# Optimization experiments

Measured on AMD Instinct MI355X. Metric: run time of the kernel, lower is better.

The kernel has to match this reference:

```python
import jax, jax.numpy as jnp
import numpy as np

N_QUBIT = 16
N_LAYERS = 4


def _rx(t):
    # RX(t) = [[cos(t/2), -i sin(t/2)], [-i sin(t/2), cos(t/2)]]; t: scalar or (B,)
    c = jnp.cos(t * 0.5) + 0j
    s = -1j * jnp.sin(t * 0.5)
    return jnp.stack([jnp.stack([c, s], -1), jnp.stack([s, c], -1)], -2)


def _ry(t):
    c = jnp.cos(t * 0.5) + 0j
    s = jnp.sin(t * 0.5) + 0j
    return jnp.stack([jnp.stack([c, -s], -1), jnp.stack([s, c], -1)], -2)


def _rz(t):
    p = jnp.exp(-0.5j * t)
    z = jnp.zeros_like(p)
    return jnp.stack([jnp.stack([p, z], -1), jnp.stack([z, jnp.conj(p)], -1)], -2)


def _apply_1q(state, U, wire, n):
    # state: (B, 2**n); U: (2,2) shared or (B,2,2) per-sample. Wire 0 = MSB.
    B = state.shape[0]
    L, R = 2 ** wire, 2 ** (n - wire - 1)
    s = state.reshape(B, L, 2, R)
    if U.ndim == 3:
        s = jnp.einsum('bij,bljr->blir', U, s)
    else:
        s = jnp.einsum('ij,bljr->blir', U, s)
    return s.reshape(B, 2 ** n)


def _apply_cnot(state, c, t, n):
    # CNOT control c, target t (flip target where control bit = 1)
    B = state.shape[0]
    a, b = (c, t) if c < t else (t, c)
    L, M, R = 2 ** a, 2 ** (b - a - 1), 2 ** (n - b - 1)
    s = state.reshape(B, L, 2, M, 2, R)
    if c < t:
        s0 = s[:, :, 0]                       # (B, L, M, 2, R)
        s1 = jnp.flip(s[:, :, 1], axis=3)     # flip target bit
        s = jnp.stack([s0, s1], axis=2)
    else:
        s0 = s[:, :, :, :, 0]                 # (B, L, 2, M, R)
        s1 = jnp.flip(s[:, :, :, :, 1], axis=2)
        s = jnp.stack([s0, s1], axis=4)
    return s.reshape(B, 2 ** n)


def setup_inputs() -> dict:
    key = jax.random.key(0)
    k1, k2 = jax.random.split(key)
    X = jax.random.normal(k1, (512, N_QUBIT), dtype=jnp.float32)
    weights = (np.pi * jax.random.uniform(k2, (N_LAYERS, N_QUBIT, 3))).astype(jnp.float32)
    bias = jnp.zeros((1,), dtype=jnp.float32)
    return {"X": X, "weights": weights, "bias": bias}


def reference(X, weights, bias):
    B, n = X.shape
    state = jnp.zeros((B, 2 ** n), jnp.complex64).at[:, 0].set(1.0)
    enc_angles = 2.0 * jnp.arctan(X)  # (B, n)
    for l in range(N_LAYERS):
        # encoder: RX(2*arctan(x_w)) on wire w (per-sample angles)
        for w in range(n):
            state = _apply_1q(state, _rx(enc_angles[:, w]), w, n)
        # single StronglyEntanglingLayers layer: Rot(phi,theta,omega) = RZ(phi) -> RY(theta) -> RZ(omega)
        for w in range(n):
            state = _apply_1q(state, _rz(weights[l, w, 0]), w, n)
            state = _apply_1q(state, _ry(weights[l, w, 1]), w, n)
            state = _apply_1q(state, _rz(weights[l, w, 2]), w, n)
        # entangler: ring of CNOTs with range r=1 (single-layer default)
        for w in range(n):
            state = _apply_cnot(state, w, (w + 1) % n, n)
    # <Z_0>: wire 0 is the most significant bit
    probs = jnp.abs(state.reshape(B, 2, -1)) ** 2
    z = probs[:, 0].sum(-1) - probs[:, 1].sum(-1)  # (B,)
    return z[:, None].astype(jnp.float32) + bias   # (B, 1), matches torch.stack of (scalar + bias)
```

## Files before the change

### kernel.cpp

```cpp
#include <hip/hip_runtime.h>
#include <hip/hip_fp16.h>
#include <cstdint>
#include <cstring>


struct BundleMeta {
    uint16_t voff[16];
    uint16_t row[4];
    uint16_t flip[4];
    uint8_t  piv[4];
    uint8_t  gidx[4];
    uint8_t  nl[4];
};

struct PassMeta {
    int       nbundles;
    BundleMeta bd[24];
    uint8_t   gap[4];
    uint8_t   nlw[4];
    uint8_t   wire_of_bit[12];
    uint16_t  meas_row;
    uint8_t   meas_nl;
};

struct Sched { int np; PassMeta pms[8]; };

constexpr Sched build_sched() {
    Sched S{};
    const int MAXP = 8;
    uint16_t D[16]{}, R[16]{};
    for (int w = 0; w < 16; ++w) { D[w] = R[w] = (uint16_t)(1u << w); }
    uint16_t gD[48]{}, gR[48]{}; uint8_t ggi[48]{}; bool gk[48]{};
    int ng = 0;
    for (int l = 1; l <= 3; ++l) {
        for (int w = 0; w < 16; ++w) { int t = (w + 1) & 15; D[w] ^= D[t]; R[t] ^= R[w]; }
        for (int w = 0; w < 16; ++w) {
            gD[ng] = D[w]; gR[ng] = R[w]; ggi[ng] = (uint8_t)(l * 16 + w);
            gk[ng] = true; ++ng;
        }
    }
    for (int w = 0; w < 16; ++w) { int t = (w + 1) & 15; D[w] ^= D[t]; R[t] ^= R[w]; }
    const uint16_t Rmeas = R[0];
    {
        uint16_t keptD[49]{}, keptR[49]{}; int nk = 0;
        keptD[nk] = 0; keptR[nk] = Rmeas; ++nk;
        for (int i = ng - 1; i >= 0; --i) {
            bool comm = true;
            for (int k = 0; k < nk; ++k) {
                if (__builtin_parity((unsigned)(gD[i] & keptR[k])) ||
                    __builtin_parity((unsigned)(keptD[k] & gR[i]))) { comm = false; break; }
            }
            if (comm) gk[i] = false;
            else { keptD[nk] = gD[i]; keptR[nk] = gR[i]; ++nk; }
        }
    }
    int nkept = 0; unsigned long long keptM = 0;
    for (int i = 0; i < ng; ++i) if (gk[i]) { ++nkept; keptM |= 1ull << i; }
    unsigned long long cm[48]{};
    for (int i = 0; i < ng; ++i)
        for (int j = 0; j < ng; ++j)
            if (!(__builtin_parity((unsigned)(gD[i] & gR[j])) ||
                  __builtin_parity((unsigned)(gD[j] & gR[i]))))
                cm[i] |= 1ull << j;
    int passOf[48]{};
    for (int i = 0; i < ng; ++i) passOf[i] = -1;
    auto bitsim = [&](uint16_t SA_, uint16_t SB_, int maxnp, int* po) -> int {
        unsigned long long sc = 0; int rem = nkept, npp = 0, stall = 0;
        while (rem > 0 && npp < MAXP) {
            uint16_t Sm = (npp & 1) ? SB_ : SA_;
            int got = 0;
            for (int i = 0; i < ng; ++i) {
                unsigned long long bi = 1ull << i;
                if (!(keptM & bi) || (sc & bi)) continue;
                if (gD[i] & Sm) continue;
                unsigned long long prior = keptM & ~sc & (bi - 1ull);
                if (prior & ~cm[i]) continue;
                sc |= bi; --rem; ++got;
                if (po) po[i] = npp;
            }
            ++npp;
            if (!got) { if (++stall >= 2) break; } else stall = 0;
            if (rem > 0 && npp >= maxnp) return 99;
        }
        return rem == 0 ? npp : 99;
    };
    int bestA = -1, bestB = 0;
    for (int target = 2; target <= MAXP && bestA < 0; ++target)
        for (int a = 0; a < 16 && bestA < 0; ++a)
            for (int b = 0; b < 16; ++b) {
                uint16_t SA_ = 0, SB_ = 0;
                for (int k = 0; k < 4; ++k) {
                    SA_ |= (uint16_t)(1u << ((a + k) & 15));
                    SB_ |= (uint16_t)(1u << ((b + k) & 15));
                }
                int rv = bitsim(SA_, SB_, target, nullptr);
                if (rv <= target) { bestA = a; bestB = b; break; }
            }
    if (bestA < 0) { bestA = 0; bestB = 8; }
    uint16_t SA = 0, SB = 0;
    int exA[4]{}, exB[4]{};
    for (int k = 0; k < 4; ++k) {
        exA[k] = (bestA + k) & 15; exB[k] = (bestB + k) & 15;
        SA |= (uint16_t)(1u << exA[k]); SB |= (uint16_t)(1u << exB[k]);
    }
    int np = bitsim(SA, SB, MAXP, passOf);
    if (np > MAXP) np = MAXP;
    if (np < 2) np = 2;
    int wireToPos[16]{}; bool used[16]{};
    int pos = 15;
    for (int k = 0; k < 4; ++k) { wireToPos[exA[k]] = pos--; used[exA[k]] = true; }
    for (int k = 0; k < 4; ++k)
        if (!used[exB[k]]) { wireToPos[exB[k]] = pos--; used[exB[k]] = true; }
    for (int w = 0; w < 16; ++w) if (!used[w]) wireToPos[w] = pos--;
    int posToWire[16]{};
    for (int w = 0; w < 16; ++w) posToWire[wireToPos[w]] = w;
    for (int p = 0; p < np; ++p) {
        PassMeta& M = S.pms[p];
        const int* ex = (p & 1) ? exB : exA;
        int gp[4]{}, gw[4]{};
        for (int k = 0; k < 4; ++k) { gp[k] = wireToPos[ex[k]]; gw[k] = ex[k]; }
        for (int a2 = 0; a2 < 4; ++a2)
            for (int b2 = a2 + 1; b2 < 4; ++b2)
                if (gp[b2] < gp[a2]) {
                    int t = gp[a2]; gp[a2] = gp[b2]; gp[b2] = t;
                    t = gw[a2]; gw[a2] = gw[b2]; gw[b2] = t;
                }
        for (int k = 0; k < 4; ++k) { M.gap[k] = (uint8_t)gp[k]; M.nlw[k] = (uint8_t)gw[k]; }
        int packedOfWire[16]{};
        for (int w = 0; w < 16; ++w) packedOfWire[w] = -1;
        int t = 0;
        for (int q = 0; q < 16; ++q) {
            bool isgap = false;
            for (int k = 0; k < 4; ++k) if (q == gp[k]) isgap = true;
            if (isgap) continue;
            M.wire_of_bit[t] = (uint8_t)posToWire[q];
            packedOfWire[posToWire[q]] = t;
            ++t;
        }
        uint16_t lm[48]{}, lr[48]{}; uint8_t lnl[48]{}, lgx[48]{}; int nsel = 0;
        for (int i = 0; i < ng; ++i) {
            if (!gk[i] || passOf[i] != p) continue;
            uint16_t m = 0, r = 0; uint8_t nl = 0;
            for (int w = 0; w < 16; ++w) {
                if ((gD[i] >> w) & 1) m |= (uint16_t)(1u << packedOfWire[w]);
                if (((gR[i] >> w) & 1) && packedOfWire[w] >= 0)
                    r |= (uint16_t)(1u << packedOfWire[w]);
            }
            for (int k = 0; k < 4; ++k)
                if ((gR[i] >> gw[k]) & 1) nl |= (uint8_t)(1u << k);
            lm[nsel] = m; lr[nsel] = r; lnl[nsel] = nl; lgx[nsel] = ggi[i]; ++nsel;
        }
        M.nbundles = 0;
        int s = 0;
        while (s < nsel && M.nbundles < 24) {
            BundleMeta& B = M.bd[M.nbundles]; ++M.nbundles;
            for (int j = 0; j < 4; ++j) {
                B.gidx[j] = 0xFF; B.row[j] = 0; B.flip[j] = 0; B.nl[j] = 0;
            }
            uint16_t red[4]{}, om[4]{}; int pv[4]{}; int nsl = 0;
            while (nsl < 4 && s < nsel) {
                uint16_t r0 = lm[s];
                for (int j = 0; j < nsl; ++j)
                    if ((r0 >> pv[j]) & 1) r0 ^= red[j];
                if (!r0) break;
                pv[nsl] = 31 - __builtin_clz((unsigned)r0);
                red[nsl] = r0; om[nsl] = lm[s];
                B.gidx[nsl] = lgx[s]; B.row[nsl] = lr[s]; B.nl[nsl] = lnl[s];
                ++nsl; ++s;
            }
            for (int b = 11; b >= 0 && nsl < 4; --b) {
                uint16_t r0 = (uint16_t)(1u << b);
                for (int j = 0; j < nsl; ++j)
                    if ((r0 >> pv[j]) & 1) r0 ^= red[j];
                if (!r0) continue;
                pv[nsl] = 31 - __builtin_clz((unsigned)r0);
                red[nsl] = r0; om[nsl] = (uint16_t)(1u << b);
                ++nsl;
            }
            for (int tt = 0; tt < 16; ++tt) {
                uint16_t v = 0;
                for (int j = 0; j < 4; ++j) if ((tt >> j) & 1) v ^= om[j];
                B.voff[tt] = v;
            }
            for (int j = 0; j < 4; ++j) {
                if (B.gidx[j] == 0xFF) continue;
                uint16_t f = 0;
                for (int tt = 0; tt < 16; ++tt)
                    if (__builtin_parity((unsigned)(B.voff[tt] & B.row[j])))
                        f |= (uint16_t)(1u << tt);
                B.flip[j] = f;
            }
            for (int a2 = 0; a2 < 4; ++a2)
                for (int b2 = a2 + 1; b2 < 4; ++b2)
                    if (pv[b2] < pv[a2]) { int tt = pv[a2]; pv[a2] = pv[b2]; pv[b2] = tt; }
            for (int j = 0; j < 4; ++j) B.piv[j] = (uint8_t)pv[j];
        }
        {
            uint16_t r = 0; uint8_t nl = 0;
            for (int w = 0; w < 16; ++w)
                if (((Rmeas >> w) & 1) && packedOfWire[w] >= 0)
                    r |= (uint16_t)(1u << packedOfWire[w]);
            for (int k = 0; k < 4; ++k)
                if ((Rmeas >> gw[k]) & 1) nl |= (uint8_t)(1u << k);
            M.meas_row = r; M.meas_nl = nl;
        }
    }
    S.np = np;
    return S;
}

constexpr Sched SCHED = build_sched();

typedef _Float16 h2 __attribute__((ext_vector_type(2)));

__device__ __forceinline__ float2 cmul2(float2 a, float2 b) {
    return make_float2(a.x * b.x - a.y * b.y, a.x * b.y + a.y * b.x);
}
__device__ __forceinline__ h2 pkfma(h2 a, h2 b, h2 c) {
    return __builtin_bit_cast(h2, __hfma2(__builtin_bit_cast(__half2, a),
                                          __builtin_bit_cast(__half2, b),
                                          __builtin_bit_cast(__half2, c)));
}
__device__ __forceinline__ h2 h2x(h2 a, unsigned m) {
    return __builtin_bit_cast(h2, __builtin_bit_cast(unsigned, a) ^ m);
}
__device__ __forceinline__ h2 bch2(unsigned u) { return __builtin_bit_cast(h2, u); }
__device__ __forceinline__ float xorf(float a, unsigned s) {
    return __uint_as_float(__float_as_uint(a) ^ s);
}
__device__ __forceinline__ unsigned pkh2(float lo, float hi) {
    h2 v; v.x = (_Float16)lo; v.y = (_Float16)hi;
    return __builtin_bit_cast(unsigned, v);
}

__device__ __forceinline__ void pair_rot(unsigned& np_, unsigned& nq_,
    unsigned p, unsigned q, unsigned AR, unsigned AIt, unsigned BRt, unsigned BI)
{
    unsigned a, b;
    asm("v_pk_mul_f16 %0, %1, %3\n\t"
        "v_pk_fma_f16 %0, %2, %3, %0 op_sel:[0,1,0] op_sel_hi:[1,0,1] neg_lo:[1,0,0]\n\t"
        "v_pk_fma_f16 %0, %4, %5, %0\n\t"
        "v_pk_fma_f16 %0, %6, %5, %0 op_sel:[0,1,0] op_sel_hi:[1,0,1] neg_lo:[1,0,0]"
        : "=&v"(a)
        : "v"(AR), "v"(AIt), "v"(p), "v"(BRt), "v"(q), "v"(BI));
    asm("v_pk_mul_f16 %0, %1, %5\n\t"
        "v_pk_fma_f16 %0, %2, %5, %0 op_sel:[0,1,0] op_sel_hi:[1,0,1] neg_hi:[1,0,0]\n\t"
        "v_pk_fma_f16 %0, %4, %3, %0 neg_lo:[1,0,0] neg_hi:[1,0,0]\n\t"
        "v_pk_fma_f16 %0, %6, %3, %0 op_sel:[0,1,0] op_sel_hi:[1,0,1] neg_lo:[1,0,0]"
        : "=&v"(b)
        : "v"(AR), "v"(AIt), "v"(p), "v"(BRt), "v"(q), "v"(BI));
    np_ = a; nq_ = b;
}

__global__ __launch_bounds__(512)
void precompute_kernel(const float* __restrict__ X, const float* __restrict__ Wt,
                       const float* __restrict__ Bs, uint4* __restrict__ Ug,
                       float* __restrict__ out)
{
    int id = blockIdx.x * 512 + threadIdx.x;
    if (id >= 512 * 64) return;
    int b = id >> 6, lw = id & 63, l = lw >> 4, w = lw & 15;
    float x  = X[b * 16 + w];
    float ce = 1.0f / sqrtf(1.0f + x * x);
    float se = x * ce;
    float t0 = 0.5f * Wt[(l * 16 + w) * 3 + 0];
    float t1 = 0.5f * Wt[(l * 16 + w) * 3 + 1];
    float t2 = 0.5f * Wt[(l * 16 + w) * 3 + 2];
    float c1 = cosf(t1), s1 = sinf(t1);
    float ca = cosf(t0 + t2), sa = sinf(t0 + t2);
    float cb = cosf(t2 - t0), sb = sinf(t2 - t0);
    float2 W00 = make_float2( c1 * ca, -c1 * sa);
    float2 W01 = make_float2(-s1 * cb,  s1 * sb);
    float2 a  = make_float2(W00.x * ce + W01.y * se, W00.y * ce - W01.x * se);
    float2 bb = make_float2(W00.y * se + W01.x * ce, -W00.x * se + W01.y * ce);
    uint4 o;
    o.x = pkh2(a.x,  a.x);
    o.y = pkh2(a.y,  a.y);
    o.z = pkh2(bb.x, bb.x);
    o.w = pkh2(bb.y, bb.y);
    Ug[id] = o;
    if (lw == 0) out[b] = Bs[0];
}

template <int P>
__global__ __launch_bounds__(256, 8)
void pass_kernel(const uint4* __restrict__ Ug, unsigned* __restrict__ state,
                 float* __restrict__ out)
{
    static constexpr PassMeta M = SCHED.pms[P];
    constexpr int NP   = SCHED.np;
    constexpr int MODE = (P == 0) ? 0 : ((P == NP - 1) ? 2 : 1);

    __shared__ __align__(16) unsigned amp[4096];
    __shared__ uint4 coef[64];
    const int tid = threadIdx.x;
    const int bb  = blockIdx.x >> 4;
    const unsigned c = blockIdx.x & 15u;
    const size_t base = (size_t)bb << 16;
    if (tid < 64) coef[tid] = Ug[(size_t)bb * 64 + tid];

    auto expand = [&](unsigned x) -> unsigned {
        #pragma unroll
        for (int k = 0; k < 4; ++k) {
            const unsigned g = M.gap[k];
            x = ((x >> g) << (g + 1)) | (x & ((1u << g) - 1u)) | (((c >> k) & 1u) << g);
        }
        return x;
    };

    if constexpr (MODE == 0) {
        __syncthreads();
        if (tid == 0) {
            float2 kv = make_float2(1.f, 0.f);
            #pragma unroll
            for (int t = 0; t < 4; ++t) {
                uint4 u = coef[M.nlw[t]];
                float ar = (float)bch2(u.x).x, ai = (float)bch2(u.y).x;
                float br = (float)bch2(u.z).x, bi = (float)bch2(u.w).x;
                float2 col = ((c >> t) & 1u) ? make_float2(-br, bi)
                                             : make_float2(ar, ai);
                kv = cmul2(kv, col);
            }
            amp[0] = pkh2(kv.x, kv.y);
        }
        __syncthreads();
        #pragma unroll
        for (int s = 0; s < 12; ++s) {
            const int n = 1 << s;
            uint4 cf = coef[M.wire_of_bit[s]];
            const h2 AR2  = bch2(cf.x);
            const h2 AIpm = h2x(bch2(cf.y), 0x00008000u);
            const h2 BRn  = h2x(bch2(cf.z), 0x80008000u);
            const h2 BIpm = h2x(bch2(cf.w), 0x00008000u);
            for (int i = tid; i < n; i += 256) {
                h2 a = bch2(amp[i]);
                h2 sw = a.yx;
                amp[i + n] = __builtin_bit_cast(unsigned, pkfma(BRn, a, BIpm * sw));
                amp[i]     = __builtin_bit_cast(unsigned, pkfma(AR2, a, AIpm * sw));
            }
            __syncthreads();
        }
    } else {
        #pragma unroll
        for (int it = 0; it < 4; ++it) {
            unsigned u = (unsigned)(tid + it * 256) * 4u;
            unsigned a = expand(u);
            uint4 v = *reinterpret_cast<const uint4*>(state + base + a);
            *reinterpret_cast<uint4*>(&amp[u]) = v;
        }
        __syncthreads();
    }

    #pragma unroll
    for (int ci = 0; ci < M.nbundles; ++ci) {
        unsigned r = (unsigned)tid;
        #pragma unroll
        for (int k = 0; k < 4; ++k) {
            const unsigned p = M.bd[ci].piv[k];
            r = ((r >> p) << (p + 1)) | (r & ((1u << p) - 1u));
        }
        const unsigned rb = r << 2;
        unsigned a_[16];
        #pragma unroll
        for (int t = 0; t < 16; ++t)
            a_[t] = *(const unsigned*)((const char*)amp +
                     (rb ^ ((unsigned)M.bd[ci].voff[t] << 2)));
        #pragma unroll
        for (int g = 0; g < 4; ++g) {
            if (M.bd[ci].gidx[g] == 0xFF) continue;
            const uint4 cf = coef[M.bd[ci].gidx[g]];
            const unsigned par = ((unsigned)__popc(r & (unsigned)M.bd[ci].row[g]) +
                                  (unsigned)__popc((unsigned)M.bd[ci].nl[g] & c)) & 1u;
            const unsigned gm = par ? 0x80008000u : 0u;
            const unsigned AR  = cf.x;
            const unsigned BI  = cf.w;
            const unsigned AIg = cf.y ^ gm;
            const unsigned BRg = cf.z ^ gm;
            const unsigned AIf = AIg ^ 0x80008000u;
            const unsigned BRf = BRg ^ 0x80008000u;
            #pragma unroll
            for (int t = 0; t < 16; ++t) {
                if (t & (1 << g)) continue;
                const int t2 = t | (1 << g);
                const bool FB = ((M.bd[ci].flip[g] >> t) & 1u) != 0;
                unsigned np_, nq_;
                pair_rot(np_, nq_, a_[t], a_[t2], AR,
                         FB ? AIf : AIg, FB ? BRf : BRg, BI);
                a_[t] = np_; a_[t2] = nq_;
            }
        }
        if (MODE == 2 && ci == M.nbundles - 1) {
            float acc = 0.f;
            const unsigned sb = (((unsigned)__popc(r & (unsigned)M.meas_row) +
                                  (unsigned)__popc((unsigned)M.meas_nl & c)) & 1u) << 31;
            #pragma unroll
            for (int t = 0; t < 16; ++t) {
                h2 a = bch2(a_[t]);
                float vr = (float)a.x, vi = (float)a.y;
                float pr = __builtin_fmaf(vr, vr, vi * vi);
                const unsigned st =
                    __builtin_parity((unsigned)(M.bd[ci].voff[t] & M.meas_row))
                        ? 0x80000000u : 0u;
                acc += xorf(pr, sb ^ st);
            }
            for (int off = 32; off > 0; off >>= 1) acc += __shfl_down(acc, off, 64);
            if ((tid & 63) == 0) atomicAdd(&out[bb], acc);
            return;
        }
        #pragma unroll
        for (int t = 0; t < 16; ++t)
            *(unsigned*)((char*)amp + (rb ^ ((unsigned)M.bd[ci].voff[t] << 2))) = a_[t];
        __syncthreads();
    }

    if constexpr (MODE == 2) {
        float acc = 0.f;
        const unsigned mcp = (unsigned)(__popc((unsigned)M.meas_nl & c) & 1);
        for (int k = 0; k < 16; ++k) {
            unsigned u = (unsigned)(tid + k * 256);
            h2 a = bch2(amp[u]);
            float vr = (float)a.x, vi = (float)a.y;
            float pr = __builtin_fmaf(vr, vr, vi * vi);
            acc += (((unsigned)__popc(u & (unsigned)M.meas_row) & 1u) ^ mcp)
                 ? -pr : pr;
        }
        for (int off = 32; off > 0; off >>= 1) acc += __shfl_down(acc, off, 64);
        if ((tid & 63) == 0) atomicAdd(&out[bb], acc);
    } else {
        #pragma unroll
        for (int it = 0; it < 4; ++it) {
            unsigned u = (unsigned)(tid + it * 256) * 4u;
            unsigned ad = expand(u);
            uint4 v = *reinterpret_cast<const uint4*>(&amp[u]);
            *reinterpret_cast<uint4*>(state + base + ad) = v;
        }
    }
}

extern "C" void kernel_launch(void* const* d_in, const int* in_sizes, int n_in,
                              void* d_out, int out_size, void* d_ws, size_t ws_size,
                              hipStream_t stream)
{
    const float* X  = (const float*)d_in[0];
    const float* Wt = (const float*)d_in[1];
    const float* Bs = (const float*)d_in[2];
    float* out = (float*)d_out;

    const size_t UG_BYTES = (size_t)512 * 64 * sizeof(uint4);
    uint4*    Ug    = (uint4*)d_ws;
    unsigned* state = (unsigned*)((char*)d_ws + UG_BYTES);
    size_t avail = ws_size > UG_BYTES ? ws_size - UG_BYTES : 0;
    int group = 1;
    while (group < 512 && (size_t)(group * 2) * 262144ull <= avail)
        group <<= 1;
    const int ngroups = 512 / group;

    constexpr int NP = SCHED.np;

    precompute_kernel<<<dim3(64), dim3(512), 0, stream>>>(X, Wt, Bs, Ug, out);
    for (int g = 0; g < ngroups; ++g) {
        const uint4* ug = Ug + (size_t)g * group * 64;
        float* og = out + (size_t)g * group;
        dim3 grid((unsigned)(group << 4));
        for (int p = 0; p < NP; ++p) {
            switch (p) {
            case 0: pass_kernel<0><<<grid, dim3(256), 0, stream>>>(ug, state, og); break;
            case 1: pass_kernel<1><<<grid, dim3(256), 0, stream>>>(ug, state, og); break;
            case 2: pass_kernel<2><<<grid, dim3(256), 0, stream>>>(ug, state, og); break;
            case 3: pass_kernel<3><<<grid, dim3(256), 0, stream>>>(ug, state, og); break;
            case 4: pass_kernel<4><<<grid, dim3(256), 0, stream>>>(ug, state, og); break;
            case 5: pass_kernel<5><<<grid, dim3(256), 0, stream>>>(ug, state, og); break;
            case 6: pass_kernel<6><<<grid, dim3(256), 0, stream>>>(ug, state, og); break;
            case 7: pass_kernel<7><<<grid, dim3(256), 0, stream>>>(ug, state, og); break;
            }
        }
    }

    (void)in_sizes; (void)n_in; (void)out_size; (void)ws_size;
}
```

Before: 330.1 us.

## Pack more gates per register bundle and build initial product state in parallel

```diff
diff --git a/kernel.cpp b/kernel.cpp
--- a/kernel.cpp
+++ b/kernel.cpp
@@ -4,18 +4,26 @@
 #include <cstring>
 
 
+struct GateC {
+    uint16_t row;
+    uint16_t flip;
+    uint8_t  mt;
+    uint8_t  nl;
+    uint8_t  gidx;
+    uint8_t  pad;
+};
+
 struct BundleMeta {
     uint16_t voff[16];
-    uint16_t row[4];
-    uint16_t flip[4];
     uint8_t  piv[4];
-    uint8_t  gidx[4];
-    uint8_t  nl[4];
+    uint8_t  ngates;
+    uint8_t  pad[3];
+    GateC    gc[24];
 };
 
 struct PassMeta {
     int       nbundles;
-    BundleMeta bd[24];
+    BundleMeta bd[8];
     uint8_t   gap[4];
     uint8_t   nlw[4];
     uint8_t   wire_of_bit[12];
@@ -151,49 +159,57 @@
             lm[nsel] = m; lr[nsel] = r; lnl[nsel] = nl; lgx[nsel] = ggi[i]; ++nsel;
         }
         M.nbundles = 0;
-        int s = 0;
-        while (s < nsel && M.nbundles < 24) {
+        int i = 0;
+        while (i < nsel && M.nbundles < 8) {
             BundleMeta& B = M.bd[M.nbundles]; ++M.nbundles;
-            for (int j = 0; j < 4; ++j) {
-                B.gidx[j] = 0xFF; B.row[j] = 0; B.flip[j] = 0; B.nl[j] = 0;
-            }
-            uint16_t red[4]{}, om[4]{}; int pv[4]{}; int nsl = 0;
-            while (nsl < 4 && s < nsel) {
-                uint16_t r0 = lm[s];
-                for (int j = 0; j < nsl; ++j)
-                    if ((r0 >> pv[j]) & 1) r0 ^= red[j];
-                if (!r0) break;
-                pv[nsl] = 31 - __builtin_clz((unsigned)r0);
-                red[nsl] = r0; om[nsl] = lm[s];
-                B.gidx[nsl] = lgx[s]; B.row[nsl] = lr[s]; B.nl[nsl] = lnl[s];
-                ++nsl; ++s;
-            }
-            for (int b = 11; b >= 0 && nsl < 4; --b) {
-                uint16_t r0 = (uint16_t)(1u << b);
-                for (int j = 0; j < nsl; ++j)
-                    if ((r0 >> pv[j]) & 1) r0 ^= red[j];
-                if (!r0) continue;
-                pv[nsl] = 31 - __builtin_clz((unsigned)r0);
-                red[nsl] = r0; om[nsl] = (uint16_t)(1u << b);
-                ++nsl;
+            uint16_t om[4]{}, red[4]{}; int pv[4]{}; uint8_t comb[4]{};
+            int rank = 0, ngate = 0;
+            while (i < nsel && ngate < 24) {
+                uint16_t x = lm[i]; uint8_t rep = 0;
+                for (int j = 0; j < rank; ++j)
+                    if ((x >> pv[j]) & 1) { x ^= red[j]; rep ^= comb[j]; }
+                if (x == 0) {
+                    B.gc[ngate].mt = rep;
+                    B.gc[ngate].row = lr[i]; B.gc[ngate].nl = lnl[i];
+                    B.gc[ngate].gidx = lgx[i];
+                    ++ngate; ++i;
+                } else if (rank < 4) {
+                    om[rank] = lm[i]; red[rank] = x;
+                    pv[rank] = 31 - __builtin_clz((unsigned)x);
+                    comb[rank] = (uint8_t)((1u << rank) | rep);
+                    B.gc[ngate].mt = (uint8_t)(1u << rank);
+                    B.gc[ngate].row = lr[i]; B.gc[ngate].nl = lnl[i];
+                    B.gc[ngate].gidx = lgx[i];
+                    ++ngate; ++i; ++rank;
+                } else break;
+            }
+            B.ngates = (uint8_t)ngate;
+            for (int b = 11; b >= 0 && rank < 4; --b) {
+                uint16_t x = (uint16_t)(1u << b);
+                for (int j = 0; j < rank; ++j)
+                    if ((x >> pv[j]) & 1) x ^= red[j];
+                if (!x) continue;
+                om[rank] = (uint16_t)(1u << b); red[rank] = x;
+                pv[rank] = 31 - __builtin_clz((unsigned)x);
+                ++rank;
             }
             for (int tt = 0; tt < 16; ++tt) {
                 uint16_t v = 0;
                 for (int j = 0; j < 4; ++j) if ((tt >> j) & 1) v ^= om[j];
                 B.voff[tt] = v;
             }
-            for (int j = 0; j < 4; ++j) {
-                if (B.gidx[j] == 0xFF) continue;
+            for (int g2 = 0; g2 < ngate; ++g2) {
                 uint16_t f = 0;
                 for (int tt = 0; tt < 16; ++tt)
-                    if (__builtin_parity((unsigned)(B.voff[tt] & B.row[j])))
+                    if (__builtin_parity((unsigned)(B.voff[tt] & B.gc[g2].row)))
                         f |= (uint16_t)(1u << tt);
-                B.flip[j] = f;
-            }
+                B.gc[g2].flip = f;
+            }
+            int sp[4] = {pv[0], pv[1], pv[2], pv[3]};
             for (int a2 = 0; a2 < 4; ++a2)
                 for (int b2 = a2 + 1; b2 < 4; ++b2)
-                    if (pv[b2] < pv[a2]) { int tt = pv[a2]; pv[a2] = pv[b2]; pv[b2] = tt; }
-            for (int j = 0; j < 4; ++j) B.piv[j] = (uint8_t)pv[j];
+                    if (sp[b2] < sp[a2]) { int tt = sp[a2]; sp[a2] = sp[b2]; sp[b2] = tt; }
+            for (int j = 0; j < 4; ++j) B.piv[j] = (uint8_t)sp[j];
         }
         {
             uint16_t r = 0; uint8_t nl = 0;
@@ -310,22 +326,29 @@
 
     if constexpr (MODE == 0) {
         __syncthreads();
-        if (tid == 0) {
-            float2 kv = make_float2(1.f, 0.f);
-            #pragma unroll
-            for (int t = 0; t < 4; ++t) {
-                uint4 u = coef[M.nlw[t]];
-                float ar = (float)bch2(u.x).x, ai = (float)bch2(u.y).x;
-                float br = (float)bch2(u.z).x, bi = (float)bch2(u.w).x;
-                float2 col = ((c >> t) & 1u) ? make_float2(-br, bi)
-                                             : make_float2(ar, ai);
-                kv = cmul2(kv, col);
-            }
-            amp[0] = pkh2(kv.x, kv.y);
-        }
+        float2 kv = make_float2(1.f, 0.f);
+        #pragma unroll
+        for (int t = 0; t < 4; ++t) {
+            uint4 u = coef[M.nlw[t]];
+            float ar = (float)bch2(u.x).x, ai = (float)bch2(u.y).x;
+            float br = (float)bch2(u.z).x, bi = (float)bch2(u.w).x;
+            float2 col = ((c >> t) & 1u) ? make_float2(-br, bi)
+                                         : make_float2(ar, ai);
+            kv = cmul2(kv, col);
+        }
+        #pragma unroll
+        for (int b = 0; b < 8; ++b) {
+            uint4 u = coef[M.wire_of_bit[b]];
+            float ar = (float)bch2(u.x).x, ai = (float)bch2(u.y).x;
+            float br = (float)bch2(u.z).x, bi = (float)bch2(u.w).x;
+            float2 col = (((unsigned)tid >> b) & 1u) ? make_float2(-br, bi)
+                                                     : make_float2(ar, ai);
+            kv = cmul2(kv, col);
+        }
+        amp[tid] = pkh2(kv.x, kv.y);
         __syncthreads();
         #pragma unroll
-        for (int s = 0; s < 12; ++s) {
+        for (int s = 8; s < 12; ++s) {
             const int n = 1 << s;
             uint4 cf = coef[M.wire_of_bit[s]];
             const h2 AR2  = bch2(cf.x);
@@ -366,11 +389,11 @@
             a_[t] = *(const unsigned*)((const char*)amp +
                      (rb ^ ((unsigned)M.bd[ci].voff[t] << 2)));
         #pragma unroll
-        for (int g = 0; g < 4; ++g) {
-            if (M.bd[ci].gidx[g] == 0xFF) continue;
-            const uint4 cf = coef[M.bd[ci].gidx[g]];
-            const unsigned par = ((unsigned)__popc(r & (unsigned)M.bd[ci].row[g]) +
-                                  (unsigned)__popc((unsigned)M.bd[ci].nl[g] & c)) & 1u;
+        for (int gi = 0; gi < M.bd[ci].ngates; ++gi) {
+            const uint4 cf = coef[M.bd[ci].gc[gi].gidx];
+            const unsigned par =
+                ((unsigned)__popc(r & (unsigned)M.bd[ci].gc[gi].row) +
+                 (unsigned)__popc((unsigned)M.bd[ci].gc[gi].nl & c)) & 1u;
             const unsigned gm = par ? 0x80008000u : 0u;
             const unsigned AR  = cf.x;
             const unsigned BI  = cf.w;
@@ -378,11 +401,13 @@
             const unsigned BRg = cf.z ^ gm;
             const unsigned AIf = AIg ^ 0x80008000u;
             const unsigned BRf = BRg ^ 0x80008000u;
+            const int mt = M.bd[ci].gc[gi].mt;
+            const int mh = 1 << (31 - __builtin_clz((unsigned)mt));
             #pragma unroll
             for (int t = 0; t < 16; ++t) {
-                if (t & (1 << g)) continue;
-                const int t2 = t | (1 << g);
-                const bool FB = ((M.bd[ci].flip[g] >> t) & 1u) != 0;
+                if (t & mh) continue;
+                const int t2 = t ^ mt;
+                const bool FB = ((M.bd[ci].gc[gi].flip >> t) & 1u) != 0;
                 unsigned np_, nq_;
                 pair_rot(np_, nq_, a_[t], a_[t2], AR,
                          FB ? AIf : AIg, FB ? BRf : BRg, BI);
```

After: 332.2 us. Within noise of the previous version (+0.6%).
